# Optimization experiments

Measured on AMD Instinct MI355X. Metric: run time of the kernel, lower is better.

Reference implementation:

```python
import jax, jax.numpy as jnp
import numpy as np

EPS = 1e-5

def layer_norm(x, gamma, beta):
    mu = jnp.mean(x, axis=-1, keepdims=True)
    var = jnp.var(x, axis=-1, keepdims=True)
    return (x - mu) * jax.lax.rsqrt(var + EPS) * gamma + beta

def setup_inputs() -> dict:
    key = jax.random.key(0)
    ks = jax.random.split(key, 9)
    B, S, H = 4, 4096, 1024
    x = jax.random.normal(ks[0], (B, S, H), dtype=jnp.float32)
    w1 = jax.random.normal(ks[1], (H, 4 * H), dtype=jnp.float32) * (1.0 / np.sqrt(H))
    b1 = jnp.zeros((4 * H,), dtype=jnp.float32)
    w2 = jax.random.normal(ks[2], (4 * H, H), dtype=jnp.float32) * (1.0 / np.sqrt(4 * H))
    b2 = jnp.zeros((H,), dtype=jnp.float32)
    g1 = jnp.ones((H,), dtype=jnp.float32)
    be1 = jnp.zeros((H,), dtype=jnp.float32)
    g2 = jnp.ones((H,), dtype=jnp.float32)
    be2 = jnp.zeros((H,), dtype=jnp.float32)
    return {"x": x, "w1": w1, "b1": b1, "w2": w2, "b2": b2,
            "g1": g1, "be1": be1, "g2": g2, "be2": be2}

def reference(x, w1, b1, w2, b2, g1, be1, g2, be2):
    # FNet mixing: FFT over hidden dim, then seq dim, take real part
    x_ft = jnp.fft.fft(jnp.fft.fft(x.astype(jnp.float32), axis=-1), axis=-2).real
    h = layer_norm(x + x_ft, g1, be1)
    # FFN with exact GELU (torch nn.GELU default); dropout is identity in eval
    ffn = jax.nn.gelu(h @ w1 + b1, approximate=False) @ w2 + b2
    return layer_norm(h + ffn, g2, be2)
```

## Files before the change

kernel.cpp:

```cpp
#include <hip/hip_runtime.h>
#include <math.h>
#include <stdint.h>

#define DI __device__ __forceinline__
typedef unsigned short u16;
typedef unsigned int   u32;
typedef unsigned long long u64;

typedef __attribute__((ext_vector_type(4))) float f32x4;
typedef __attribute__((ext_vector_type(8))) short bf16x8;

DI float bf2f(u16 v){ return __uint_as_float(((u32)v) << 16); }
DI u16 f2bf(float f){ u32 u = __float_as_uint(f); return (u16)((u + 0x7FFFu + ((u >> 16) & 1u)) >> 16); }
DI u32 pack2(float re, float im){ return (u32)f2bf(re) | ((u32)f2bf(im) << 16); }

DI float gelu_fast(float v){
  float t = v * v;
  float z = v * fmaf(0.0356774081f, t, 0.7978845608f);
  z = fminf(z, 15.0f);
  float e = __expf(2.0f * z);
  return v * e * __frcp_rn(1.0f + e);
}

__global__ __launch_bounds__(256) void transpose_u32(const u32* __restrict__ in, u32* __restrict__ out, int R, int C){
  __shared__ u32 tile[64][65];
  int t = threadIdx.x;
  int c = t & 63, r0 = t >> 6;
  size_t bofs = (size_t)blockIdx.z * (size_t)R * (size_t)C;
  const u32* ib = in  + bofs + (size_t)(blockIdx.y * 64) * C + blockIdx.x * 64;
  u32*       ob = out + bofs + (size_t)(blockIdx.x * 64) * R + blockIdx.y * 64;
  #pragma unroll
  for (int i = 0; i < 16; i++){ int r = r0 + i * 4; tile[r][c] = ib[(size_t)r * C + c]; }
  __syncthreads();
  #pragma unroll
  for (int i = 0; i < 16; i++){ int r = r0 + i * 4; ob[(size_t)r * R + c] = tile[c][r]; }
}

__global__ __launch_bounds__(256) void transpose_f32_bf16(const float* __restrict__ in, u16* __restrict__ out, int R, int C){
  __shared__ u16 tile[64][65];
  int t = threadIdx.x;
  int c = t & 63, r0 = t >> 6;
  const float* ib = in  + (size_t)(blockIdx.y * 64) * C + blockIdx.x * 64;
  u16*         ob = out + (size_t)(blockIdx.x * 64) * R + blockIdx.y * 64;
  #pragma unroll
  for (int i = 0; i < 16; i++){ int r = r0 + i * 4; tile[r][c] = f2bf(ib[(size_t)r * C + c]); }
  __syncthreads();
  #pragma unroll
  for (int i = 0; i < 16; i++){ int r = r0 + i * 4; ob[(size_t)r * R + c] = tile[c][r]; }
}

template<int LOGN>
DI float2* fft_r4(float2* s, float2* d, int t){
  const int Q = 1 << (LOGN - 2);
  #pragma unroll
  for (int st = 0; st < (LOGN >> 1); ++st){
    const int m = 1 << (2 * st);
    const float ang = -6.28318530717958647692f * (float)m / (float)(1 << LOGN);
    #pragma unroll
    for (int j0 = 0; j0 < Q; j0 += 256){
      int j = j0 + t;
      int p = j >> (2 * st);
      int q = j & (m - 1);
      int o = q + (p << (2 * st + 2));
      float2 a0 = s[j], a1 = s[j + Q], a2 = s[j + 2 * Q], a3 = s[j + 3 * Q];
      float s0r = a0.x + a2.x, s0i = a0.y + a2.y, d0r = a0.x - a2.x, d0i = a0.y - a2.y;
      float s1r = a1.x + a3.x, s1i = a1.y + a3.y, d1r = a1.x - a3.x, d1i = a1.y - a3.y;
      float sn, cs; __sincosf(ang * (float)p, &sn, &cs);
      float t2r = cs * cs - sn * sn, t2i = 2.f * cs * sn;
      float t3r = t2r * cs - t2i * sn, t3i = t2r * sn + t2i * cs;
      float e1r = d0r + d1i, e1i = d0i - d1r;
      float e2r = s0r - s1r, e2i = s0i - s1i;
      float e3r = d0r - d1i, e3i = d0i + d1r;
      d[o]         = make_float2(s0r + s1r, s0i + s1i);
      d[o + m]     = make_float2(cs * e1r - sn * e1i,  cs * e1i + sn * e1r);
      d[o + 2 * m] = make_float2(t2r * e2r - t2i * e2i, t2r * e2i + t2i * e2r);
      d[o + 3 * m] = make_float2(t3r * e3r - t3i * e3i, t3r * e3i + t3i * e3r);
    }
    __syncthreads();
    float2* tp = s; s = d; d = tp;
  }
  return s;
}

__global__ __launch_bounds__(256) void fft_seq(const float* __restrict__ xT, u32* __restrict__ ZT2,
                                               float* __restrict__ Zny){
  __shared__ float2 A[4096], Bb[4096];
  int t = threadIdx.x, g = blockIdx.x;
  const float* r0 = xT + (size_t)(2 * g) * 4096;
  #pragma unroll
  for (int i = 0; i < 4; i++){
    int idx = i * 1024 + t * 4;
    float4 va = *(const float4*)(r0 + idx);
    float4 vb = *(const float4*)(r0 + 4096 + idx);
    A[idx + 0] = make_float2(va.x, vb.x);
    A[idx + 1] = make_float2(va.y, vb.y);
    A[idx + 2] = make_float2(va.z, vb.z);
    A[idx + 3] = make_float2(va.w, vb.w);
  }
  __syncthreads();
  float2* R = fft_r4<12>(A, Bb, t);
  size_t ob0 = (size_t)(2 * g) * 2048;
  #pragma unroll
  for (int i = 0; i < 2; i++){
    int k0 = i * 1024 + t * 4;
    u32 wa[4], wb[4];
    #pragma unroll
    for (int kk = 0; kk < 4; kk++){
      int k = k0 + kk, m = (4096 - k) & 4095;
      float2 zk = R[k], zm = R[m];
      wa[kk] = pack2(0.5f * (zk.x + zm.x), 0.5f * (zk.y - zm.y));
      wb[kk] = pack2(0.5f * (zk.y + zm.y), 0.5f * (zm.x - zk.x));
    }
    *(uint4*)(ZT2 + ob0 + k0)        = make_uint4(wa[0], wa[1], wa[2], wa[3]);
    *(uint4*)(ZT2 + ob0 + 2048 + k0) = make_uint4(wb[0], wb[1], wb[2], wb[3]);
  }
  if (t == 0){ float2 z = R[2048]; Zny[2 * g] = z.x; Zny[2 * g + 1] = z.y; }
}

DI void block_stats4(float a1, float a2, float b1, float b2, int t,
                     float& mA, float& iA, float& mB, float& iB){
  __shared__ float sh[4][4];
  #pragma unroll
  for (int o = 32; o > 0; o >>= 1){
    a1 += __shfl_down(a1, o); a2 += __shfl_down(a2, o);
    b1 += __shfl_down(b1, o); b2 += __shfl_down(b2, o);
  }
  if ((t & 63) == 0){ int w = t >> 6; sh[w][0] = a1; sh[w][1] = a2; sh[w][2] = b1; sh[w][3] = b2; }
  __syncthreads();
  float SA = sh[0][0] + sh[1][0] + sh[2][0] + sh[3][0];
  float QA = sh[0][1] + sh[1][1] + sh[2][1] + sh[3][1];
  float SB = sh[0][2] + sh[1][2] + sh[2][2] + sh[3][2];
  float QB = sh[0][3] + sh[1][3] + sh[2][3] + sh[3][3];
  mA = SA * (1.f / 1024.f); iA = rsqrtf(QA * (1.f / 1024.f) - mA * mA + 1e-5f);
  mB = SB * (1.f / 1024.f); iB = rsqrtf(QB * (1.f / 1024.f) - mB * mB + 1e-5f);
}

__global__ __launch_bounds__(256) void fft_hid_ln(const u32* __restrict__ Z2, const float* __restrict__ Zny,
    const float* __restrict__ x, const float* __restrict__ g1, const float* __restrict__ be1,
    u16* __restrict__ h){
  __shared__ float2 A[1024], Bb[1024];
  int t = threadIdx.x, id = blockIdx.x;
  int b = id / 2049, k = id - b * 2049;
  int idx = t * 4;
  if (k == 2048){
    float4 v = *(const float4*)(Zny + b * 1024 + idx);
    A[idx + 0] = make_float2(v.x, 0.f); A[idx + 1] = make_float2(v.y, 0.f);
    A[idx + 2] = make_float2(v.z, 0.f); A[idx + 3] = make_float2(v.w, 0.f);
  } else {
    uint4 zv = *(const uint4*)(Z2 + ((size_t)b * 2048 + k) * 1024 + idx);
    A[idx + 0] = make_float2(bf2f((u16)(zv.x & 0xffffu)), bf2f((u16)(zv.x >> 16)));
    A[idx + 1] = make_float2(bf2f((u16)(zv.y & 0xffffu)), bf2f((u16)(zv.y >> 16)));
    A[idx + 2] = make_float2(bf2f((u16)(zv.z & 0xffffu)), bf2f((u16)(zv.z >> 16)));
    A[idx + 3] = make_float2(bf2f((u16)(zv.w & 0xffffu)), bf2f((u16)(zv.w >> 16)));
  }
  __syncthreads();
  float2* R = fft_r4<10>(A, Bb, t);
  int rowA = b * 4096 + k;
  bool two = (k >= 1) && (k <= 2047);
  int rowB = b * 4096 + (4096 - k);
  float4 xa = *(const float4*)(x + (size_t)rowA * 1024 + idx);
  float vA0 = R[idx + 0].x + xa.x, vA1 = R[idx + 1].x + xa.y;
  float vA2 = R[idx + 2].x + xa.z, vA3 = R[idx + 3].x + xa.w;
  float vB0 = 0.f, vB1 = 0.f, vB2 = 0.f, vB3 = 0.f;
  if (two){
    float4 xb = *(const float4*)(x + (size_t)rowB * 1024 + idx);
    vB0 = R[(1024 - (idx + 0)) & 1023].x + xb.x;
    vB1 = R[(1024 - (idx + 1)) & 1023].x + xb.y;
    vB2 = R[(1024 - (idx + 2)) & 1023].x + xb.z;
    vB3 = R[(1024 - (idx + 3)) & 1023].x + xb.w;
  }
  float mA, iA, mB, iB;
  block_stats4(vA0 + vA1 + vA2 + vA3, vA0 * vA0 + vA1 * vA1 + vA2 * vA2 + vA3 * vA3,
               vB0 + vB1 + vB2 + vB3, vB0 * vB0 + vB1 * vB1 + vB2 * vB2 + vB3 * vB3,
               t, mA, iA, mB, iB);
  float4 gv = *(const float4*)(g1 + idx);
  float4 bv = *(const float4*)(be1 + idx);
  ushort4 oA;
  oA.x = f2bf((vA0 - mA) * iA * gv.x + bv.x);
  oA.y = f2bf((vA1 - mA) * iA * gv.y + bv.y);
  oA.z = f2bf((vA2 - mA) * iA * gv.z + bv.z);
  oA.w = f2bf((vA3 - mA) * iA * gv.w + bv.w);
  *(ushort4*)(h + (size_t)rowA * 1024 + idx) = oA;
  if (two){
    ushort4 oB;
    oB.x = f2bf((vB0 - mB) * iB * gv.x + bv.x);
    oB.y = f2bf((vB1 - mB) * iB * gv.y + bv.y);
    oB.z = f2bf((vB2 - mB) * iB * gv.z + bv.z);
    oB.w = f2bf((vB3 - mB) * iB * gv.w + bv.w);
    *(ushort4*)(h + (size_t)rowB * 1024 + idx) = oB;
  }
}

__global__ __launch_bounds__(256) void ln_rows(const u16* __restrict__ yv, const float* __restrict__ g,
    const float* __restrict__ be, float* __restrict__ o){
  int t = threadIdx.x;
  size_t base = (size_t)blockIdx.x * 1024;
  int idx = t * 4;
  ushort4 v4 = *(const ushort4*)(yv + base + idx);
  float v0 = bf2f(v4.x), v1 = bf2f(v4.y), v2 = bf2f(v4.z), v3 = bf2f(v4.w);
  float mA, iA, mB, iB;
  block_stats4(v0 + v1 + v2 + v3, v0 * v0 + v1 * v1 + v2 * v2 + v3 * v3, 0.f, 0.f, t, mA, iA, mB, iB);
  float4 gv = *(const float4*)(g + idx);
  float4 bv = *(const float4*)(be + idx);
  float4 ov;
  ov.x = (v0 - mA) * iA * gv.x + bv.x;
  ov.y = (v1 - mA) * iA * gv.y + bv.y;
  ov.z = (v2 - mA) * iA * gv.z + bv.z;
  ov.w = (v3 - mA) * iA * gv.w + bv.w;
  *(float4*)(o + base + idx) = ov;
}

typedef const __attribute__((address_space(1))) void* as1cp;
typedef __attribute__((address_space(3))) void* as3p;
DI void async_copy16(const void* g, void* l){
  __builtin_amdgcn_global_load_lds((as1cp)(u64)g, (as3p)(u32)(u64)l, 16, 0, 0);
}
DI void bar(){
  asm volatile("" ::: "memory");
  __builtin_amdgcn_s_barrier();
  asm volatile("" ::: "memory");
}

template<int DOGELU>
__global__ __launch_bounds__(512, 2) void gemm256(const u16* __restrict__ A, const u16* __restrict__ Bm,
    const float* __restrict__ bias, const u16* __restrict__ resid, u16* __restrict__ C,
    int M, int N, int K, int gn_shift, int npg_shift, int mpg, int bpg, int npt)
{
  __shared__ u16 sA[2][2][8192];
  __shared__ u16 sB[2][2][8192];
  int t = threadIdx.x, wv = t >> 6, ln = t & 63;

  int bid = blockIdx.x;
  int c8 = bid & 7, j0 = bid >> 3;
  int ng = c8 & ((1 << gn_shift) - 1);
  int mg = c8 >> gn_shift;
  int npg_m1 = (1 << npg_shift) - 1;

  int wm = wv >> 2, wn = wv & 3;
  int lt = ln & 15;
  int cs = (((ln >> 4) ^ ((ln >> 1) & 3)) << 3);
  int arow = (wm * 128 + lt) * 32 + cs;
  int brow = (wn * 64 + lt) * 32 + cs;
  int srow = wv * 32 + (ln >> 2);
  int gch  = ((ln & 3) ^ ((srow >> 1) & 3)) << 3;
  int ldof = wv * 1024 + ln * 8;
  int NT = K >> 6;

  #define STAGE(g0, g1, kc, unit) do{ \
    async_copy16((g0) + (kc), (unit) + ldof); \
    async_copy16((g1) + (kc), (unit) + 512 + ldof); }while(0)

  for (int s = 0; s < npt; ++s){
    int jt = j0 + s * bpg;
    int n0 = (((ng << npg_shift) + (jt & npg_m1)) << 8);
    int m0 = ((mg * mpg + (jt >> npg_shift)) << 8);
    const u16* gA0 = A  + (size_t)(m0 + srow) * K + gch;
    const u16* gA1 = gA0 + (size_t)16 * K;
    const u16* gB0 = Bm + (size_t)(n0 + srow) * K + gch;
    const u16* gB1 = gB0 + (size_t)16 * K;

    f32x4 acc[8][4];
    #pragma unroll
    for (int mf = 0; mf < 8; mf++)
      #pragma unroll
      for (int nf = 0; nf < 4; nf++) acc[mf][nf] = (f32x4){0.f, 0.f, 0.f, 0.f};

    STAGE(gA0, gA1, 0,  &sA[0][0][0]);
    STAGE(gB0, gB1, 0,  &sB[0][0][0]);
    STAGE(gA0, gA1, 32, &sA[0][1][0]);
    STAGE(gB0, gB1, 32, &sB[0][1][0]);
    STAGE(gA0, gA1, 64, &sA[1][0][0]);
    STAGE(gB0, gB1, 64, &sB[1][0][0]);
    STAGE(gA0, gA1, 96, &sA[1][1][0]);
    asm volatile("s_waitcnt vmcnt(6)" ::: "memory");
    bar();

    for (int kt = 0; kt < NT; ++kt){
      int buf = kt & 1;
      u16* a0s = &sA[buf][0][0];
      u16* a1s = &sA[buf][1][0];
      u16* b0s = &sB[buf][0][0];
      u16* b1s = &sB[buf][1][0];
      u16* bn1 = &sB[buf ^ 1][1][0];
      bool st1 = (kt + 1) < NT;
      bool st2 = (kt + 2) < NT;
      int kb1 = (kt + 1) << 6, kb2 = (kt + 2) << 6;
      bf16x8 af[8], b0r, b1r, b2r, b3r;

      #pragma unroll
      for (int mf = 0; mf < 8; mf++) af[mf] = *(const bf16x8*)(a0s + arow + mf * 512);
      b0r = *(const bf16x8*)(b0s + brow);
      b1r = *(const bf16x8*)(b0s + brow + 512);
      if (st1) STAGE(gB0, gB1, kb1 + 32, bn1);
      bar();
      __builtin_amdgcn_s_setprio(1);
      #pragma unroll
      for (int mf = 0; mf < 8; mf++){
        acc[mf][0] = __builtin_amdgcn_mfma_f32_16x16x32_bf16(af[mf], b0r, acc[mf][0], 0, 0, 0);
        acc[mf][1] = __builtin_amdgcn_mfma_f32_16x16x32_bf16(af[mf], b1r, acc[mf][1], 0, 0, 0);
      }
      __builtin_amdgcn_s_setprio(0);
      bar();

      b2r = *(const bf16x8*)(b0s + brow + 1024);
      b3r = *(const bf16x8*)(b0s + brow + 1536);
      if (st2) STAGE(gA0, gA1, kb2, a0s);
      bar();
      __builtin_amdgcn_s_setprio(1);
      #pragma unroll
      for (int mf = 0; mf < 8; mf++){
        acc[mf][2] = __builtin_amdgcn_mfma_f32_16x16x32_bf16(af[mf], b2r, acc[mf][2], 0, 0, 0);
        acc[mf][3] = __builtin_amdgcn_mfma_f32_16x16x32_bf16(af[mf], b3r, acc[mf][3], 0, 0, 0);
      }
      __builtin_amdgcn_s_setprio(0);
      bar();

      #pragma unroll
      for (int mf = 0; mf < 8; mf++) af[mf] = *(const bf16x8*)(a1s + arow + mf * 512);
      b0r = *(const bf16x8*)(b1s + brow);
      b1r = *(const bf16x8*)(b1s + brow + 512);
      if (st2) STAGE(gB0, gB1, kb2, b0s);
      bar();
      __builtin_amdgcn_s_setprio(1);
      #pragma unroll
      for (int mf = 0; mf < 8; mf++){
        acc[mf][0] = __builtin_amdgcn_mfma_f32_16x16x32_bf16(af[mf], b0r, acc[mf][0], 0, 0, 0);
        acc[mf][1] = __builtin_amdgcn_mfma_f32_16x16x32_bf16(af[mf], b1r, acc[mf][1], 0, 0, 0);
      }
      __builtin_amdgcn_s_setprio(0);
      bar();

      b2r = *(const bf16x8*)(b1s + brow + 1024);
      b3r = *(const bf16x8*)(b1s + brow + 1536);
      if (st2) STAGE(gA0, gA1, kb2 + 32, a1s);
      bar();
      __builtin_amdgcn_s_setprio(1);
      #pragma unroll
      for (int mf = 0; mf < 8; mf++){
        acc[mf][2] = __builtin_amdgcn_mfma_f32_16x16x32_bf16(af[mf], b2r, acc[mf][2], 0, 0, 0);
        acc[mf][3] = __builtin_amdgcn_mfma_f32_16x16x32_bf16(af[mf], b3r, acc[mf][3], 0, 0, 0);
      }
      __builtin_amdgcn_s_setprio(0);
      if (st2) asm volatile("s_waitcnt vmcnt(6)" ::: "memory");
      else     asm volatile("s_waitcnt vmcnt(0)" ::: "memory");
      bar();
    }

    int colq = lt, rq = ln >> 4;
    #pragma unroll
    for (int mf = 0; mf < 8; mf++){
      int mr = m0 + wm * 128 + mf * 16 + rq * 4;
      #pragma unroll
      for (int nf = 0; nf < 4; nf++){
        int col = n0 + wn * 64 + nf * 16 + colq;
        float bv = bias[col];
        #pragma unroll
        for (int i = 0; i < 4; i++){
          float v = acc[mf][nf][i] + bv;
          if (DOGELU){
            v = gelu_fast(v);
          } else {
            v += bf2f(resid[(size_t)(mr + i) * N + col]);
          }
          C[(size_t)(mr + i) * N + col] = f2bf(v);
        }
      }
    }
  }
  #undef STAGE
}

static inline int ilog2(int v){ int s = 0; while ((1 << s) < v) ++s; return s; }

extern "C" void kernel_launch(void* const* d_in, const int* in_sizes, int n_in,
                              void* d_out, int out_size, void* d_ws, size_t ws_size,
                              hipStream_t stream){
  const float* x   = (const float*)d_in[0];
  const float* w1  = (const float*)d_in[1];
  const float* b1  = (const float*)d_in[2];
  const float* w2  = (const float*)d_in[3];
  const float* b2  = (const float*)d_in[4];
  const float* g1  = (const float*)d_in[5];
  const float* be1 = (const float*)d_in[6];
  const float* g2  = (const float*)d_in[7];
  const float* be2 = (const float*)d_in[8];
  float* out = (float*)d_out;
  char* ws = (char*)d_ws;
  const size_t MB = (size_t)1 << 20;
  float* xT  = (float*)(ws);
  u32*  ZT2  = (u32*)(ws + 64 * MB);
  float* Zny = (float*)(ws + 96 * MB);
  u32*  Z2   = (u32*)(ws);
  u16*  h    = (u16*)(ws + 32 * MB);
  u16*  w1T  = (u16*)(ws + 64 * MB);
  u16*  w2T  = (u16*)(ws + 72 * MB);
  u16*  u    = (u16*)(ws + 80 * MB);
  u16*  y    = (u16*)(ws);
  dim3 blk(256, 1, 1);
  dim3 blk2(512, 1, 1);

  transpose_u32<<<dim3(16, 64, 4), blk, 0, stream>>>((const u32*)x, (u32*)xT, 4096, 1024);
  fft_seq      <<<dim3(2048, 1, 1), blk, 0, stream>>>(xT, ZT2, Zny);
  transpose_u32<<<dim3(32, 16, 4), blk, 0, stream>>>(ZT2, Z2, 1024, 2048);
  fft_hid_ln   <<<dim3(4 * 2049, 1, 1), blk, 0, stream>>>(Z2, Zny, x, g1, be1, h);

  transpose_f32_bf16<<<dim3(64, 16, 1), blk, 0, stream>>>(w1, w1T, 1024, 4096);
  transpose_f32_bf16<<<dim3(16, 64, 1), blk, 0, stream>>>(w2, w2T, 4096, 1024);
  int nch = (ws_size >= (size_t)209 * MB) ? 1 : (ws_size >= (size_t)145 * MB) ? 2 : 4;
  int Mc = 16384 / nch;
  for (int ch = 0; ch < nch; ++ch){
    const u16* hch = h + (size_t)ch * Mc * 1024;
    u16* ych = y + (size_t)ch * Mc * 1024;
    {
      int tm = Mc >> 8, tn = 16, gn = 2;
      int tiles = tm * tn;
      int grid = tiles < 256 ? tiles : 256;
      int npt = tiles / grid, bpg = grid >> 3;
      int npgs = ilog2(tn >> gn);
      int mpg = tm >> (3 - gn);
      gemm256<1><<<dim3(grid), blk2, 0, stream>>>(hch, w1T, b1, (const u16*)nullptr, u,
                                                  Mc, 4096, 1024, gn, npgs, mpg, bpg, npt);
    }
    {
      int tm = Mc >> 8, tn = 4, gn = 0;
      int tiles = tm * tn;
      int grid = tiles < 256 ? tiles : 256;
      int npt = tiles / grid, bpg = grid >> 3;
      int npgs = ilog2(tn >> gn);
      int mpg = tm >> (3 - gn);
      gemm256<0><<<dim3(grid), blk2, 0, stream>>>(u, w2T, b2, hch, ych,
                                                  Mc, 1024, 4096, gn, npgs, mpg, bpg, npt);
    }
  }
  ln_rows<<<dim3(16384, 1, 1), blk, 0, stream>>>(y, g2, be2, out);
}
```

Before: 552.2 us.

## Prefetch next tile's prologue during epilogue and restructure LDS fragment loads

```diff
diff --git a/kernel.cpp b/kernel.cpp
--- a/kernel.cpp
+++ b/kernel.cpp
@@ -249,31 +249,32 @@
   #define STAGE(g0, g1, kc, unit) do{ \
     async_copy16((g0) + (kc), (unit) + ldof); \
     async_copy16((g1) + (kc), (unit) + 512 + ldof); }while(0)
+  #define PROLOGUE() do{ \
+    STAGE(gA0, gA1, 0,  &sA[0][0][0]); \
+    STAGE(gB0, gB1, 0,  &sB[0][0][0]); \
+    STAGE(gA0, gA1, 32, &sA[0][1][0]); \
+    STAGE(gB0, gB1, 32, &sB[0][1][0]); \
+    STAGE(gA0, gA1, 64, &sA[1][0][0]); \
+    STAGE(gB0, gB1, 64, &sB[1][0][0]); \
+    STAGE(gA0, gA1, 96, &sA[1][1][0]); }while(0)
+
+  int jt = j0;
+  int n0 = (((ng << npg_shift) + (jt & npg_m1)) << 8);
+  int m0 = ((mg * mpg + (jt >> npg_shift)) << 8);
+  const u16* gA0 = A  + (size_t)(m0 + srow) * K + gch;
+  const u16* gA1 = gA0 + (size_t)16 * K;
+  const u16* gB0 = Bm + (size_t)(n0 + srow) * K + gch;
+  const u16* gB1 = gB0 + (size_t)16 * K;
+  PROLOGUE();
+  asm volatile("s_waitcnt vmcnt(6)" ::: "memory");
+  bar();
 
   for (int s = 0; s < npt; ++s){
-    int jt = j0 + s * bpg;
-    int n0 = (((ng << npg_shift) + (jt & npg_m1)) << 8);
-    int m0 = ((mg * mpg + (jt >> npg_shift)) << 8);
-    const u16* gA0 = A  + (size_t)(m0 + srow) * K + gch;
-    const u16* gA1 = gA0 + (size_t)16 * K;
-    const u16* gB0 = Bm + (size_t)(n0 + srow) * K + gch;
-    const u16* gB1 = gB0 + (size_t)16 * K;
-
     f32x4 acc[8][4];
     #pragma unroll
     for (int mf = 0; mf < 8; mf++)
       #pragma unroll
       for (int nf = 0; nf < 4; nf++) acc[mf][nf] = (f32x4){0.f, 0.f, 0.f, 0.f};
-
-    STAGE(gA0, gA1, 0,  &sA[0][0][0]);
-    STAGE(gB0, gB1, 0,  &sB[0][0][0]);
-    STAGE(gA0, gA1, 32, &sA[0][1][0]);
-    STAGE(gB0, gB1, 32, &sB[0][1][0]);
-    STAGE(gA0, gA1, 64, &sA[1][0][0]);
-    STAGE(gB0, gB1, 64, &sB[1][0][0]);
-    STAGE(gA0, gA1, 96, &sA[1][1][0]);
-    asm volatile("s_waitcnt vmcnt(6)" ::: "memory");
-    bar();
 
     for (int kt = 0; kt < NT; ++kt){
       int buf = kt & 1;
@@ -285,60 +286,57 @@
       bool st1 = (kt + 1) < NT;
       bool st2 = (kt + 2) < NT;
       int kb1 = (kt + 1) << 6, kb2 = (kt + 2) << 6;
-      bf16x8 af[8], b0r, b1r, b2r, b3r;
-
-      #pragma unroll
-      for (int mf = 0; mf < 8; mf++) af[mf] = *(const bf16x8*)(a0s + arow + mf * 512);
-      b0r = *(const bf16x8*)(b0s + brow);
-      b1r = *(const bf16x8*)(b0s + brow + 512);
+      bf16x8 af1[8], af2[8], b1r[4], b2r[4];
+
+      #pragma unroll
+      for (int mf = 0; mf < 8; mf++) af1[mf] = *(const bf16x8*)(a0s + arow + mf * 512);
+      #pragma unroll
+      for (int nf = 0; nf < 4; nf++) b1r[nf] = *(const bf16x8*)(b0s + brow + nf * 512);
       if (st1) STAGE(gB0, gB1, kb1 + 32, bn1);
       bar();
       __builtin_amdgcn_s_setprio(1);
       #pragma unroll
       for (int mf = 0; mf < 8; mf++){
-        acc[mf][0] = __builtin_amdgcn_mfma_f32_16x16x32_bf16(af[mf], b0r, acc[mf][0], 0, 0, 0);
-        acc[mf][1] = __builtin_amdgcn_mfma_f32_16x16x32_bf16(af[mf], b1r, acc[mf][1], 0, 0, 0);
+        acc[mf][0] = __builtin_amdgcn_mfma_f32_16x16x32_bf16(af1[mf], b1r[0], acc[mf][0], 0, 0, 0);
+        acc[mf][1] = __builtin_amdgcn_mfma_f32_16x16x32_bf16(af1[mf], b1r[1], acc[mf][1], 0, 0, 0);
       }
       __builtin_amdgcn_s_setprio(0);
       bar();
 
-      b2r = *(const bf16x8*)(b0s + brow + 1024);
-      b3r = *(const bf16x8*)(b0s + brow + 1536);
+      #pragma unroll
+      for (int mf = 0; mf < 8; mf++) af2[mf] = *(const bf16x8*)(a1s + arow + mf * 512);
+      #pragma unroll
+      for (int nf = 0; nf < 4; nf++) b2r[nf] = *(const bf16x8*)(b1s + brow + nf * 512);
       if (st2) STAGE(gA0, gA1, kb2, a0s);
       bar();
       __builtin_amdgcn_s_setprio(1);
       #pragma unroll
       for (int mf = 0; mf < 8; mf++){
-        acc[mf][2] = __builtin_amdgcn_mfma_f32_16x16x32_bf16(af[mf], b2r, acc[mf][2], 0, 0, 0);
-        acc[mf][3] = __builtin_amdgcn_mfma_f32_16x16x32_bf16(af[mf], b3r, acc[mf][3], 0, 0, 0);
+        acc[mf][2] = __builtin_amdgcn_mfma_f32_16x16x32_bf16(af1[mf], b1r[2], acc[mf][2], 0, 0, 0);
+        acc[mf][3] = __builtin_amdgcn_mfma_f32_16x16x32_bf16(af1[mf], b1r[3], acc[mf][3], 0, 0, 0);
       }
       __builtin_amdgcn_s_setprio(0);
-      bar();
-
-      #pragma unroll
-      for (int mf = 0; mf < 8; mf++) af[mf] = *(const bf16x8*)(a1s + arow + mf * 512);
-      b0r = *(const bf16x8*)(b1s + brow);
-      b1r = *(const bf16x8*)(b1s + brow + 512);
+      asm volatile("s_waitcnt lgkmcnt(0)" ::: "memory");
+      bar();
+
       if (st2) STAGE(gB0, gB1, kb2, b0s);
       bar();
       __builtin_amdgcn_s_setprio(1);
       #pragma unroll
       for (int mf = 0; mf < 8; mf++){
-        acc[mf][0] = __builtin_amdgcn_mfma_f32_16x16x32_bf16(af[mf], b0r, acc[mf][0], 0, 0, 0);
-        acc[mf][1] = __builtin_amdgcn_mfma_f32_16x16x32_bf16(af[mf], b1r, acc[mf][1], 0, 0, 0);
+        acc[mf][0] = __builtin_amdgcn_mfma_f32_16x16x32_bf16(af2[mf], b2r[0], acc[mf][0], 0, 0, 0);
+        acc[mf][1] = __builtin_amdgcn_mfma_f32_16x16x32_bf16(af2[mf], b2r[1], acc[mf][1], 0, 0, 0);
       }
       __builtin_amdgcn_s_setprio(0);
       bar();
 
-      b2r = *(const bf16x8*)(b1s + brow + 1024);
-      b3r = *(const bf16x8*)(b1s + brow + 1536);
       if (st2) STAGE(gA0, gA1, kb2 + 32, a1s);
       bar();
       __builtin_amdgcn_s_setprio(1);
       #pragma unroll
       for (int mf = 0; mf < 8; mf++){
-        acc[mf][2] = __builtin_amdgcn_mfma_f32_16x16x32_bf16(af[mf], b2r, acc[mf][2], 0, 0, 0);
-        acc[mf][3] = __builtin_amdgcn_mfma_f32_16x16x32_bf16(af[mf], b3r, acc[mf][3], 0, 0, 0);
+        acc[mf][2] = __builtin_amdgcn_mfma_f32_16x16x32_bf16(af2[mf], b2r[2], acc[mf][2], 0, 0, 0);
+        acc[mf][3] = __builtin_amdgcn_mfma_f32_16x16x32_bf16(af2[mf], b2r[3], acc[mf][3], 0, 0, 0);
       }
       __builtin_amdgcn_s_setprio(0);
       if (st2) asm volatile("s_waitcnt vmcnt(6)" ::: "memory");
@@ -346,13 +344,25 @@
       bar();
     }
 
+    int em0 = m0, en0 = n0;
+    if (s + 1 < npt){
+      jt = j0 + (s + 1) * bpg;
+      n0 = (((ng << npg_shift) + (jt & npg_m1)) << 8);
+      m0 = ((mg * mpg + (jt >> npg_shift)) << 8);
+      gA0 = A  + (size_t)(m0 + srow) * K + gch;
+      gA1 = gA0 + (size_t)16 * K;
+      gB0 = Bm + (size_t)(n0 + srow) * K + gch;
+      gB1 = gB0 + (size_t)16 * K;
+      PROLOGUE();
+    }
+
     int colq = lt, rq = ln >> 4;
     #pragma unroll
     for (int mf = 0; mf < 8; mf++){
-      int mr = m0 + wm * 128 + mf * 16 + rq * 4;
+      int mr = em0 + wm * 128 + mf * 16 + rq * 4;
       #pragma unroll
       for (int nf = 0; nf < 4; nf++){
-        int col = n0 + wn * 64 + nf * 16 + colq;
+        int col = en0 + wn * 64 + nf * 16 + colq;
         float bv = bias[col];
         #pragma unroll
         for (int i = 0; i < 4; i++){
@@ -366,7 +376,13 @@
         }
       }
     }
-  }
+
+    if (s + 1 < npt){
+      asm volatile("s_waitcnt vmcnt(6)" ::: "memory");
+      bar();
+    }
+  }
+  #undef PROLOGUE
   #undef STAGE
 }
 
```

Result: no change. 546.6 us (-1.0%).
